# Kernel optimization log

Hardware: AMD Instinct MI355X
Metric: run time of the kernel (lower is better)

Reference implementation:

```python
import jax, jax.numpy as jnp
import numpy as np

B, S, HID, H, D, F = 8, 256, 1024, 16, 64, 64
BASE_LR = 0.1
MAX_STEPS = 4
EPS = 1e-5


def _ln(x, g, b):
    mu = jnp.mean(x, axis=-1, keepdims=True)
    var = jnp.var(x, axis=-1, keepdims=True)
    return (x - mu) * jax.lax.rsqrt(var + EPS) * g + b


def setup_inputs() -> dict:
    key = jax.random.key(0)
    ks = jax.random.split(key, 10)
    n = lambda i, shape, s=0.02: jax.random.normal(ks[i], shape, jnp.float32) * s
    return {
        "x": jax.random.normal(ks[0], (B, S, HID), jnp.float32),
        "wq": n(1, (HID, HID)),
        "wk": n(2, (HID, HID)),
        "wv": n(3, (HID, HID)),
        "fw_w1": n(4, (H, D, F), 0.05),
        "fw_b1": jnp.zeros((H, F), jnp.float32),
        "fw_w2": n(5, (H, F, D), 0.05),
        "fw_b2": jnp.zeros((H, D), jnp.float32),
        "fw_ln_g": jnp.ones((H, D), jnp.float32),
        "fw_ln_b": jnp.zeros((H, D), jnp.float32),
        "loss_w": n(6, (D, D)),
        "loss_b": jnp.zeros((D,), jnp.float32),
        "ttt_g": jnp.ones((H, D), jnp.float32),
        "ttt_b": jnp.zeros((H, D), jnp.float32),
        "wo": n(7, (HID, HID)),
        "wg": n(8, (HID, HID)),
        "pn_g": jnp.ones((HID,), jnp.float32),
        "pn_b": jnp.zeros((HID,), jnp.float32),
    }


def _fw_apply(p, kx):
    # per-head fast-weight MLP: kx (B,H,D) -> (B,H,D)
    w1, b1, w2, b2, lg, lb = p
    h = jax.nn.gelu(jnp.einsum('bhd,hdf->bhf', kx, w1) + b1)
    o = jnp.einsum('bhf,hfd->bhd', h, w2) + b2
    return _ln(o, lg, lb)


def _forward(x, wq, wk, wv, fw_w1, fw_b1, fw_w2, fw_b2, fw_ln_g, fw_ln_b,
             loss_w, loss_b, ttt_g, ttt_b, wo, wg, pn_g, pn_b):
    # projections (torch Linear with W stored as (in,out) here: y = x @ W)
    q = (x @ wq).reshape(B, S, H, D)
    k = (x @ wk).reshape(B, S, H, D)
    v = (x @ wv).reshape(B, S, H, D)
    # scan over tokens: xs shaped (S, B, H, D)
    qs = jnp.swapaxes(q, 0, 1)
    ks_ = jnp.swapaxes(k, 0, 1)
    vs = jnp.swapaxes(v, 0, 1)

    def token_step(p, qkv):
        q_t, k_t, v_t = qkv  # (B,H,D) each
        target = v_t - k_t

        def loss_fn(pp):
            z = _fw_apply(pp, k_t)
            pred = jnp.einsum('bhd,de->bhe', z, loss_w) + loss_b
            return jnp.mean((pred - target) ** 2)

        for _ in range(MAX_STEPS):
            g = jax.grad(loss_fn)(p)
            p = jax.tree.map(lambda a, gg: a - BASE_LR * gg, p, g)
        z = _fw_apply(p, k_t)
        z = _ln(z, ttt_g, ttt_b)  # per-head post-TTT LayerNorm
        return p, q_t + z

    p0 = (fw_w1, fw_b1, fw_w2, fw_b2, fw_ln_g, fw_ln_b)
    _, outs = jax.lax.scan(token_step, p0, (qs, ks_, vs))
    out = jnp.swapaxes(outs, 0, 1).reshape(B, S, HID)
    gated = jax.nn.gelu(x @ wg) * _ln(out, pn_g, pn_b)
    return gated @ wo


def reference(x, wq, wk, wv, fw_w1, fw_b1, fw_w2, fw_b2, fw_ln_g, fw_ln_b,
              loss_w, loss_b, ttt_g, ttt_b, wo, wg, pn_g, pn_b):
    return _forward(x, wq, wk, wv, fw_w1, fw_b1, fw_w2, fw_b2, fw_ln_g, fw_ln_b,
                    loss_w, loss_b, ttt_g, ttt_b, wo, wg, pn_g, pn_b)
```

## Files before the change

### kernel.cpp

```cpp
#include <hip/hip_runtime.h>

#define Bv 8
#define Sv 256
#define Hv 16
#define Dv 64
#define LR 0.1f
#define SCALE (2.0f / 8192.0f)

using bf16x8 = __attribute__((ext_vector_type(8))) short;
using bf16x4 = __attribute__((ext_vector_type(4))) short;
using f32x4  = __attribute__((ext_vector_type(4))) float;
#define MFMA16(A, B, C) __builtin_amdgcn_mfma_f32_16x16x32_bf16(A, B, C, 0, 0, 0)

constexpr int U_W1T = 0;
constexpr int U_W2T = 8704;
constexpr int U_W2R = 17408;
constexpr int U_G   = 26112;
constexpr int U_LwR = 34816;
constexpr int U_K   = 43520;
constexpr int U_H   = 45696;
constexpr int U_Z   = 47872;
constexpr int U_TG  = 50048;
constexpr int U_DO  = 52224;
constexpr int U_KT  = 54400;
constexpr int U_HT  = 55424;
constexpr int U_DOT = 56448;
constexpr int U_DAT = 57472;
constexpr int F_BASE = 29248;
constexpr int F_O   = F_BASE;
constexpr int F_XH  = F_BASE + 544;
constexpr int F_GD  = F_XH + 544;
constexpr int F_TGL = F_GD + 544;
constexpr int F_B1  = F_TGL + 544;
constexpr int F_B2  = F_B1 + 64;
constexpr int F_LG  = F_B2 + 64;
constexpr int F_LB  = F_LG + 64;
constexpr int F_C1  = F_LB + 64;
constexpr int F_TGm = F_C1 + 64;
constexpr int F_TBm = F_TGm + 64;
constexpr int F_RSTD = F_TBm + 64;
constexpr int U_KG  = (F_RSTD + 8) * 2;
constexpr int U_HT2 = U_KG + 256;
constexpr int LDS_BYTES = (U_HT2 + 1024) * 2;

__device__ __forceinline__ short bf_rn(float v) {
    unsigned u = __float_as_uint(v);
    unsigned r = u + 0x7fffu + ((u >> 16) & 1u);
    return (short)(r >> 16);
}
__device__ __forceinline__ void cvt1(float v, short &hi, short &lo) {
    hi = bf_rn(v);
    float hf = __uint_as_float(((unsigned)(unsigned short)hi) << 16);
    lo = bf_rn(v - hf);
}
__device__ __forceinline__ float bf2f(short u) {
    return __uint_as_float(((unsigned)(unsigned short)u) << 16);
}
__device__ __forceinline__ unsigned cvtpk(float a, float b) {
    unsigned r;
    asm("v_cvt_pk_bf16_f32 %0, %1, %2" : "=v"(r) : "v"(a), "v"(b));
    return r;
}
__device__ __forceinline__ void cvt2(float a, float b, unsigned &hw,
                                     unsigned &lw) {
    hw = cvtpk(a, b);
    float ra = a - __uint_as_float(hw << 16);
    float rb = b - __uint_as_float(hw & 0xffff0000u);
    lw = cvtpk(ra, rb);
}
template <int CTRL>
__device__ __forceinline__ float dpp_add(float v) {
    int s = __builtin_amdgcn_update_dpp(0, __float_as_int(v), CTRL, 0xF, 0xF,
                                        true);
    return v + __int_as_float(s);
}
__device__ __forceinline__ float red32(float v) {
    v = dpp_add<0xB1>(v);
    v = dpp_add<0x4E>(v);
    v = dpp_add<0x124>(v);
    v = dpp_add<0x128>(v);
    v += __shfl_xor(v, 16);
    return v;
}
__device__ __forceinline__ float fast_tanh(float u) {
    u = fminf(fmaxf(u, -10.f), 10.f);
    float e = __expf(2.0f * u);
    return (e - 1.0f) / (e + 1.0f);
}
__device__ __forceinline__ void gelu_both(float x, float &g, float &dg) {
    const float C0 = 0.7978845608028654f, A0 = 0.044715f;
    float x2 = x * x;
    float u = C0 * x * (1.0f + A0 * x2);
    float t = fast_tanh(u);
    g = 0.5f * x * (1.0f + t);
    float du = C0 * (1.0f + 3.0f * A0 * x2);
    dg = 0.5f * (1.0f + t) + 0.5f * x * (1.0f - t * t) * du;
}
__device__ __forceinline__ float gelu_f(float x) {
    const float C0 = 0.7978845608028654f, A0 = 0.044715f;
    float u = C0 * x * (1.0f + A0 * x * x);
    return 0.5f * x * (1.0f + fast_tanh(u));
}

__device__ __forceinline__ f32x4 mm64(const unsigned short *Ap,
                                      const unsigned short *Bp,
                                      int w, int c, int q) {
    const unsigned short *ar = Ap + c * 136 + 8 * q;
    const unsigned short *br = Bp + (16 * w + c) * 136 + 8 * q;
    bf16x8 ah0 = *(const bf16x8 *)(ar);
    bf16x8 al0 = *(const bf16x8 *)(ar + 64);
    bf16x8 bh0 = *(const bf16x8 *)(br);
    bf16x8 bl0 = *(const bf16x8 *)(br + 64);
    bf16x8 ah1 = *(const bf16x8 *)(ar + 32);
    bf16x8 al1 = *(const bf16x8 *)(ar + 96);
    bf16x8 bh1 = *(const bf16x8 *)(br + 32);
    bf16x8 bl1 = *(const bf16x8 *)(br + 96);
    f32x4 x0 = {0.f, 0.f, 0.f, 0.f}, x1 = {0.f, 0.f, 0.f, 0.f};
    x0 = MFMA16(ah0, bh0, x0); x1 = MFMA16(ah1, bh1, x1);
    x0 = MFMA16(al0, bh0, x0); x1 = MFMA16(al1, bh1, x1);
    x0 = MFMA16(ah0, bl0, x0); x1 = MFMA16(ah1, bl1, x1);
    x0 = MFMA16(al0, bl0, x0); x1 = MFMA16(al1, bl1, x1);
    return x0 + x1;
}

__device__ __forceinline__ void updW2(const bf16x8 *a4, bf16x8 b,
                                      unsigned short *WT, int w, int c,
                                      int q) {
    unsigned short *p0 = &WT[(16 * w + c) * 136 + 4 * q];
    uint2 oh[4], ol[4];
#pragma unroll
    for (int mt = 0; mt < 4; ++mt) {
        oh[mt] = *(uint2 *)(p0 + 16 * mt);
        ol[mt] = *(uint2 *)(p0 + 16 * mt + 64);
    }
    f32x4 g[4];
#pragma unroll
    for (int mt = 0; mt < 4; ++mt) {
        f32x4 z = {0.f, 0.f, 0.f, 0.f};
        g[mt] = MFMA16(a4[mt], b, z);
    }
#pragma unroll
    for (int mt = 0; mt < 4; ++mt) {
        float v0 = __uint_as_float(oh[mt].x << 16) +
                   __uint_as_float(ol[mt].x << 16) - LR * g[mt][0];
        float v1 = __uint_as_float(oh[mt].x & 0xffff0000u) +
                   __uint_as_float(ol[mt].x & 0xffff0000u) - LR * g[mt][1];
        float v2 = __uint_as_float(oh[mt].y << 16) +
                   __uint_as_float(ol[mt].y << 16) - LR * g[mt][2];
        float v3 = __uint_as_float(oh[mt].y & 0xffff0000u) +
                   __uint_as_float(ol[mt].y & 0xffff0000u) - LR * g[mt][3];
        unsigned nh0, nl0, nh1, nl1;
        cvt2(v0, v1, nh0, nl0);
        cvt2(v2, v3, nh1, nl1);
        uint2 nh, nl;
        nh.x = nh0; nh.y = nh1;
        nl.x = nl0; nl.y = nl1;
        *(uint2 *)(p0 + 16 * mt) = nh;
        *(uint2 *)(p0 + 16 * mt + 64) = nl;
    }
}

__global__ __launch_bounds__(256) void ttt_scan(
    const float *__restrict__ q_g, const float *__restrict__ k_g,
    const float *__restrict__ v_g, float *__restrict__ out_g,
    const float *__restrict__ fw_w1, const float *__restrict__ fw_b1,
    const float *__restrict__ fw_w2, const float *__restrict__ fw_b2,
    const float *__restrict__ fw_lng, const float *__restrict__ fw_lnb,
    const float *__restrict__ loss_w, const float *__restrict__ loss_bv,
    const float *__restrict__ ttt_gv, const float *__restrict__ ttt_bv) {
    extern __shared__ char smem[];
    unsigned short *us = (unsigned short *)smem;
    float *fs = (float *)smem;

    unsigned short *W1T = us + U_W1T, *W2T = us + U_W2T, *W2R = us + U_W2R;
    unsigned short *Gp = us + U_G, *LwR = us + U_LwR;
    unsigned short *Kp = us + U_K, *Hp = us + U_H, *Zp = us + U_Z;
    unsigned short *TGp = us + U_TG, *DOp = us + U_DO;
    unsigned short *KT = us + U_KT, *HT0 = us + U_HT;
    unsigned short *DOT = us + U_DOT, *DAT = us + U_DAT;
    unsigned short *KgT = us + U_KG, *HT1 = us + U_HT2;
    float *o_s = fs + F_O, *xh_s = fs + F_XH;
    float *b2_s = fs + F_B2, *lg_s = fs + F_LG;
    float *lb_s = fs + F_LB, *c1_s = fs + F_C1;
    float *tG_s = fs + F_TGm, *tB_s = fs + F_TBm, *rstd_s = fs + F_RSTD;

    const int h = blockIdx.x, tid = threadIdx.x;
    const int w = tid >> 6, lane = tid & 63, c = lane & 15, q = lane >> 4;
    const int bb = tid >> 5, j0 = (tid & 31) * 2;

    for (int i = tid; i < 4096; i += 256) {
        int r = i >> 6, cc = i & 63;
        short hi, lo;
        cvt1(fw_w1[h * 4096 + i], hi, lo);
        W1T[cc * 136 + r] = (unsigned short)hi;
        W1T[cc * 136 + 64 + r] = (unsigned short)lo;
        cvt1(fw_w2[h * 4096 + i], hi, lo);
        W2T[cc * 136 + r] = (unsigned short)hi;
        W2T[cc * 136 + 64 + r] = (unsigned short)lo;
        W2R[r * 136 + cc] = (unsigned short)hi;
        W2R[r * 136 + 64 + cc] = (unsigned short)lo;
        cvt1(loss_w[i], hi, lo);
        LwR[r * 136 + cc] = (unsigned short)hi;
        LwR[r * 136 + 64 + cc] = (unsigned short)lo;
    }
    for (int i = tid; i < 5 * 8 * 128; i += 256) {
        int a = i / 128, u = i % 128;
        int arr = a >> 3, row = 8 + (a & 7);
        unsigned short *base = (arr == 0) ? Kp : (arr == 1) ? Hp
                              : (arr == 2) ? Zp : (arr == 3) ? TGp : DOp;
        base[row * 136 + u] = 0;
    }
    __syncthreads();
#pragma unroll 1
    for (int mt = 0; mt < 4; ++mt) {
        f32x4 g = mm64(LwR + 16 * 136 * mt, LwR, w, c, q);
#pragma unroll
        for (int r = 0; r < 4; ++r) {
            short hi, lo;
            cvt1(g[r], hi, lo);
            int dr = 16 * mt + 4 * q + r, dc = 16 * w + c;
            Gp[dr * 136 + dc] = (unsigned short)hi;
            Gp[dr * 136 + 64 + dc] = (unsigned short)lo;
        }
    }
    if (tid < 64) {
        b2_s[tid] = fw_b2[h * 64 + tid];
        lg_s[tid] = fw_lng[h * 64 + tid];
        lb_s[tid] = fw_lnb[h * 64 + tid];
        tG_s[tid] = ttt_gv[h * 64 + tid];
        tB_s[tid] = ttt_bv[h * 64 + tid];
        float c1 = 0.f;
        for (int e = 0; e < 64; ++e) c1 += loss_bv[e] * loss_w[tid * 64 + e];
        c1_s[tid] = c1;
    }

    float2 pk, pv, pq, q_cur;
    {
        int idx = ((bb * Sv + 0) * Hv + h) * Dv + j0;
        float2 k0 = *(const float2 *)&k_g[idx];
        float2 v0 = *(const float2 *)&v_g[idx];
        q_cur = *(const float2 *)&q_g[idx];
        unsigned khw, klw;
        cvt2(k0.x, k0.y, khw, klw);
        *(unsigned *)&Kp[bb * 136 + j0] = khw;
        *(unsigned *)&Kp[bb * 136 + 64 + j0] = klw;
        KT[j0 * 16 + bb] = (unsigned short)khw;
        KT[j0 * 16 + 8 + bb] = (unsigned short)klw;
        KT[(j0 + 1) * 16 + bb] = (unsigned short)(khw >> 16);
        KT[(j0 + 1) * 16 + 8 + bb] = (unsigned short)(klw >> 16);
        unsigned thw, tlw;
        cvt2(v0.x - k0.x, v0.y - k0.y, thw, tlw);
        *(unsigned *)&TGp[bb * 136 + j0] = thw;
        *(unsigned *)&TGp[bb * 136 + 64 + j0] = tlw;
    }
    float b1_r = (q < 2) ? fw_b1[h * 64 + 16 * w + c] : 0.f;
    __syncthreads();
    float c1_r = c1_s[16 * w + c];
    f32x4 gd_r = {0.f, 0.f, 0.f, 0.f};
    f32x4 tgl_r = {0.f, 0.f, 0.f, 0.f};

#pragma unroll 1
    for (int t = 0; t < Sv; ++t) {
        if (t + 1 < Sv) {
            int idx2 = ((bb * Sv + t + 1) * Hv + h) * Dv + j0;
            pk = *(const float2 *)&k_g[idx2];
            pv = *(const float2 *)&v_g[idx2];
            pq = *(const float2 *)&q_g[idx2];
        }

        f32x4 acc1 = mm64(Kp, W1T, w, c, q);
        {
            f32x4 a2 = mm64(TGp, LwR, w, c, q);
            if (q < 2) {
#pragma unroll
                for (int r = 0; r < 4; ++r) tgl_r[r] = a2[r] - c1_r;
            }
        }
        if (w == 0) {
            f32x4 kg = mm64(Kp, Kp, 0, c, q);
            if (q < 2) {
#pragma unroll
                for (int r = 0; r < 4; ++r) {
                    short hi, lo;
                    cvt1(-LR * kg[r], hi, lo);
                    KgT[c * 16 + 4 * q + r] = (unsigned short)hi;
                    KgT[c * 16 + 8 + 4 * q + r] = (unsigned short)lo;
                }
            }
        }
        if (q < 2) {
            int col = 16 * w + c;
            float gv[4];
#pragma unroll
            for (int r = 0; r < 4; ++r) {
                float g, dg;
                gelu_both(acc1[r] + b1_r, g, dg);
                gv[r] = g;
                gd_r[r] = dg;
            }
            unsigned h01, l01, h23, l23;
            cvt2(gv[0], gv[1], h01, l01);
            cvt2(gv[2], gv[3], h23, l23);
            Hp[(4 * q + 0) * 136 + col] = (unsigned short)h01;
            Hp[(4 * q + 1) * 136 + col] = (unsigned short)(h01 >> 16);
            Hp[(4 * q + 2) * 136 + col] = (unsigned short)h23;
            Hp[(4 * q + 3) * 136 + col] = (unsigned short)(h23 >> 16);
            Hp[(4 * q + 0) * 136 + 64 + col] = (unsigned short)l01;
            Hp[(4 * q + 1) * 136 + 64 + col] = (unsigned short)(l01 >> 16);
            Hp[(4 * q + 2) * 136 + 64 + col] = (unsigned short)l23;
            Hp[(4 * q + 3) * 136 + 64 + col] = (unsigned short)(l23 >> 16);
            uint2 hh, hl;
            hh.x = h01; hh.y = h23;
            hl.x = l01; hl.y = l23;
            *(uint2 *)&HT0[col * 16 + 4 * q] = hh;
            *(uint2 *)&HT0[col * 16 + 8 + 4 * q] = hl;
        }
        __syncthreads();

#pragma unroll 1
        for (int step = 0; step < 4; ++step) {
            const unsigned short *HTr = (step & 1) ? HT1 : HT0;
            unsigned short *HTw = (step & 1) ? HT0 : HT1;
            f32x4 acc = mm64(Hp, W2T, w, c, q);
            if (q < 2) {
                float bias = b2_s[16 * w + c];
#pragma unroll
                for (int r = 0; r < 4; ++r)
                    o_s[(4 * q + r) * 68 + 16 * w + c] = acc[r] + bias;
            }
            __syncthreads();
            float xh0_r, xh1_r;
            {
                float2 xv = *(const float2 *)&o_s[bb * 68 + j0];
                float mu = red32(xv.x + xv.y) * (1.f / 64.f);
                float d0 = xv.x - mu, d1 = xv.y - mu;
                float var = red32(d0 * d0 + d1 * d1) * (1.f / 64.f);
                float rs = rsqrtf(var + 1e-5f);
                float xh0 = d0 * rs, xh1 = d1 * rs;
                float2 xw; xw.x = xh0; xw.y = xh1;
                *(float2 *)&xh_s[bb * 68 + j0] = xw;
                float z0 = xh0 * lg_s[j0] + lb_s[j0];
                float z1 = xh1 * lg_s[j0 + 1] + lb_s[j0 + 1];
                unsigned zh, zl;
                cvt2(z0, z1, zh, zl);
                *(unsigned *)&Zp[bb * 136 + j0] = zh;
                *(unsigned *)&Zp[bb * 136 + 64 + j0] = zl;
                if ((tid & 31) == 0) rstd_s[bb] = rs;
                xh0_r = xh0; xh1_r = xh1;
            }
            __syncthreads();
            acc = mm64(Zp, Gp, w, c, q);
            if (q < 2) {
                int col = 16 * w + c;
#pragma unroll
                for (int r = 0; r < 4; ++r)
                    o_s[(4 * q + r) * 68 + col] = (acc[r] - tgl_r[r]) * SCALE;
            }
            __syncthreads();
            {
                float2 dzv = *(const float2 *)&o_s[bb * 68 + j0];
                float dxh0 = dzv.x * lg_s[j0], dxh1 = dzv.y * lg_s[j0 + 1];
                float S1 = red32(dxh0 + dxh1) * (1.f / 64.f);
                float S2 = red32(dxh0 * xh0_r + dxh1 * xh1_r) * (1.f / 64.f);
                float rs = rstd_s[bb];
                float do0 = rs * (dxh0 - S1 - xh0_r * S2);
                float do1 = rs * (dxh1 - S1 - xh1_r * S2);
                unsigned dh, dl;
                cvt2(do0, do1, dh, dl);
                *(unsigned *)&DOp[bb * 136 + j0] = dh;
                *(unsigned *)&DOp[bb * 136 + 64 + j0] = dl;
                DOT[j0 * 16 + bb] = (unsigned short)dh;
                DOT[j0 * 16 + 8 + bb] = (unsigned short)dl;
                DOT[(j0 + 1) * 16 + bb] = (unsigned short)(dh >> 16);
                DOT[(j0 + 1) * 16 + 8 + bb] = (unsigned short)(dl >> 16);
            }
            __syncthreads();
            bf16x8 zf8;
#pragma unroll
            for (int j = 0; j < 8; ++j) zf8[j] = 0;
            bf16x8 aK[4], aH[4], aD[4];
#pragma unroll
            for (int mt = 0; mt < 4; ++mt) {
                aK[mt] = *(const bf16x8 *)&KT[(16 * mt + c) * 16 + (q & 1) * 8];
                aH[mt] = *(const bf16x8 *)&HTr[(16 * mt + c) * 16 + (q & 1) * 8];
                aD[mt] = *(const bf16x8 *)&DOT[(16 * mt + c) * 16 + (q & 1) * 8];
            }
            bf16x8 bDO = zf8, bHT = zf8;
            if (q < 2) {
                bDO = *(const bf16x8 *)&DOT[(16 * w + c) * 16];
                bHT = *(const bf16x8 *)&HTr[(16 * w + c) * 16];
            } else if (q == 2) {
                bDO = *(const bf16x8 *)&DOT[(16 * w + c) * 16 + 8];
                bHT = *(const bf16x8 *)&HTr[(16 * w + c) * 16 + 8];
            }
            bf16x8 aKg = *(const bf16x8 *)&KgT[c * 16 + (q & 1) * 8];
            acc = mm64(DOp, W2R, w, c, q);
            {
                float b1sum = 0.f;
                if (q < 2) {
                    int col = 16 * w + c;
                    float da0 = acc[0] * gd_r[0];
                    float da1 = acc[1] * gd_r[1];
                    float da2 = acc[2] * gd_r[2];
                    float da3 = acc[3] * gd_r[3];
                    b1sum = da0 + da1 + da2 + da3;
                    unsigned h01, l01, h23, l23;
                    cvt2(da0, da1, h01, l01);
                    cvt2(da2, da3, h23, l23);
                    uint2 th, tl;
                    th.x = h01; th.y = h23;
                    tl.x = l01; tl.y = l23;
                    *(uint2 *)&DAT[col * 16 + 4 * q] = th;
                    *(uint2 *)&DAT[col * 16 + 8 + 4 * q] = tl;
                }
                b1sum += __shfl_xor(b1sum, 16);
                bf16x8 bDA = zf8;
                if (q < 2)
                    bDA = *(const bf16x8 *)&DAT[(16 * w + c) * 16];
                else if (q == 2)
                    bDA = *(const bf16x8 *)&DAT[(16 * w + c) * 16 + 8];
                updW2(aK, bDA, W1T, w, c, q);
                updW2(aH, bDO, W2T, w, c, q);
                updW2(aD, bHT, W2R, w, c, q);
                if (w == 2) {
                    bf16x8 oh_ = *(const bf16x8 *)&DOT[lane * 16];
                    bf16x8 ol_ = *(const bf16x8 *)&DOT[lane * 16 + 8];
                    float db2 = 0.f;
#pragma unroll
                    for (int j = 0; j < 8; ++j)
                        db2 += bf2f(oh_[j]) + bf2f(ol_[j]);
                    b2_s[lane] -= LR * db2;
                } else if (w == 3) {
                    float dlb = 0.f, dlg = 0.f;
#pragma unroll
                    for (int b = 0; b < 8; ++b) {
                        float dzv = o_s[b * 68 + lane];
                        dlb += dzv;
                        dlg += dzv * xh_s[b * 68 + lane];
                    }
                    lb_s[lane] -= LR * dlb;
                    lg_s[lane] -= LR * dlg;
                }
                acc1 = MFMA16(aKg, bDA, acc1);
                b1_r -= LR * b1sum;
                if (q < 2) {
                    int col = 16 * w + c;
                    if (step < 3) {
                        float gv[4];
#pragma unroll
                        for (int r = 0; r < 4; ++r) {
                            float g, dg;
                            gelu_both(acc1[r] + b1_r, g, dg);
                            gv[r] = g;
                            gd_r[r] = dg;
                        }
                        unsigned h01, l01, h23, l23;
                        cvt2(gv[0], gv[1], h01, l01);
                        cvt2(gv[2], gv[3], h23, l23);
                        Hp[(4 * q + 0) * 136 + col] = (unsigned short)h01;
                        Hp[(4 * q + 1) * 136 + col] = (unsigned short)(h01 >> 16);
                        Hp[(4 * q + 2) * 136 + col] = (unsigned short)h23;
                        Hp[(4 * q + 3) * 136 + col] = (unsigned short)(h23 >> 16);
                        Hp[(4 * q + 0) * 136 + 64 + col] = (unsigned short)l01;
                        Hp[(4 * q + 1) * 136 + 64 + col] = (unsigned short)(l01 >> 16);
                        Hp[(4 * q + 2) * 136 + 64 + col] = (unsigned short)l23;
                        Hp[(4 * q + 3) * 136 + 64 + col] = (unsigned short)(l23 >> 16);
                        uint2 hh, hl;
                        hh.x = h01; hh.y = h23;
                        hl.x = l01; hl.y = l23;
                        *(uint2 *)&HTw[col * 16 + 4 * q] = hh;
                        *(uint2 *)&HTw[col * 16 + 8 + 4 * q] = hl;
                    } else {
                        float gv[4];
#pragma unroll
                        for (int r = 0; r < 4; ++r)
                            gv[r] = gelu_f(acc1[r] + b1_r);
                        unsigned h01, l01, h23, l23;
                        cvt2(gv[0], gv[1], h01, l01);
                        cvt2(gv[2], gv[3], h23, l23);
                        Hp[(4 * q + 0) * 136 + col] = (unsigned short)h01;
                        Hp[(4 * q + 1) * 136 + col] = (unsigned short)(h01 >> 16);
                        Hp[(4 * q + 2) * 136 + col] = (unsigned short)h23;
                        Hp[(4 * q + 3) * 136 + col] = (unsigned short)(h23 >> 16);
                        Hp[(4 * q + 0) * 136 + 64 + col] = (unsigned short)l01;
                        Hp[(4 * q + 1) * 136 + 64 + col] = (unsigned short)(l01 >> 16);
                        Hp[(4 * q + 2) * 136 + 64 + col] = (unsigned short)l23;
                        Hp[(4 * q + 3) * 136 + 64 + col] = (unsigned short)(l23 >> 16);
                    }
                }
            }
            __syncthreads();
        }

        f32x4 acc = mm64(Hp, W2T, w, c, q);
        if (q < 2) {
            float bias = b2_s[16 * w + c];
#pragma unroll
            for (int r = 0; r < 4; ++r)
                o_s[(4 * q + r) * 68 + 16 * w + c] = acc[r] + bias;
        }
        if (t + 1 < Sv) {
            unsigned khw, klw;
            cvt2(pk.x, pk.y, khw, klw);
            *(unsigned *)&Kp[bb * 136 + j0] = khw;
            *(unsigned *)&Kp[bb * 136 + 64 + j0] = klw;
            KT[j0 * 16 + bb] = (unsigned short)khw;
            KT[j0 * 16 + 8 + bb] = (unsigned short)klw;
            KT[(j0 + 1) * 16 + bb] = (unsigned short)(khw >> 16);
            KT[(j0 + 1) * 16 + 8 + bb] = (unsigned short)(klw >> 16);
            unsigned thw, tlw;
            cvt2(pv.x - pk.x, pv.y - pk.y, thw, tlw);
            *(unsigned *)&TGp[bb * 136 + j0] = thw;
            *(unsigned *)&TGp[bb * 136 + 64 + j0] = tlw;
        }
        __syncthreads();
        {
            float2 xv = *(const float2 *)&o_s[bb * 68 + j0];
            float mu = red32(xv.x + xv.y) * (1.f / 64.f);
            float d0 = xv.x - mu, d1 = xv.y - mu;
            float var = red32(d0 * d0 + d1 * d1) * (1.f / 64.f);
            float rs = rsqrtf(var + 1e-5f);
            float z0 = d0 * rs * lg_s[j0] + lb_s[j0];
            float z1 = d1 * rs * lg_s[j0 + 1] + lb_s[j0 + 1];
            float mu2 = red32(z0 + z1) * (1.f / 64.f);
            float e0 = z0 - mu2, e1 = z1 - mu2;
            float var2 = red32(e0 * e0 + e1 * e1) * (1.f / 64.f);
            float rs2 = rsqrtf(var2 + 1e-5f);
            float z20 = e0 * rs2 * tG_s[j0] + tB_s[j0];
            float z21 = e1 * rs2 * tG_s[j0 + 1] + tB_s[j0 + 1];
            int idx = ((bb * Sv + t) * Hv + h) * Dv + j0;
            float2 ov;
            ov.x = q_cur.x + z20;
            ov.y = q_cur.y + z21;
            *(float2 *)&out_g[idx] = ov;
            q_cur = pq;
        }
    }
}

__global__ __launch_bounds__(256) void gemm_f32(
    const float *__restrict__ A, const float *__restrict__ B,
    float *__restrict__ C, const float *__restrict__ gate_ln,
    int M, int N, int K, int mode) {
    __shared__ float As[16][68];
    __shared__ float Bs[16][64];
    const int tid = threadIdx.x;
    const int tx = tid & 15, ty = tid >> 4;
    const int bm = blockIdx.y * 64, bn = blockIdx.x * 64;

    float acc[4][4] = {};
    for (int k0 = 0; k0 < K; k0 += 16) {
        {
            int r = tid >> 2, kk = (tid & 3) * 4;
            float4 av = *(const float4 *)(A + (long)(bm + r) * K + k0 + kk);
            As[kk + 0][r] = av.x;
            As[kk + 1][r] = av.y;
            As[kk + 2][r] = av.z;
            As[kk + 3][r] = av.w;
            int rr = tid >> 4, cc = (tid & 15) * 4;
            float4 bv = *(const float4 *)(B + (long)(k0 + rr) * N + bn + cc);
            *(float4 *)&Bs[rr][cc] = bv;
        }
        __syncthreads();
#pragma unroll
        for (int kk = 0; kk < 16; ++kk) {
            float4 a4 = *(float4 *)&As[kk][ty * 4];
            float4 b4 = *(float4 *)&Bs[kk][tx * 4];
            float a[4] = {a4.x, a4.y, a4.z, a4.w};
            float b[4] = {b4.x, b4.y, b4.z, b4.w};
#pragma unroll
            for (int i = 0; i < 4; ++i)
#pragma unroll
                for (int j = 0; j < 4; ++j) acc[i][j] += a[i] * b[j];
        }
        __syncthreads();
    }
#pragma unroll
    for (int i = 0; i < 4; ++i) {
        int row = bm + ty * 4 + i;
        float4 out;
        float v[4];
#pragma unroll
        for (int j = 0; j < 4; ++j) {
            float val = acc[i][j];
            if (mode == 1) {
                int col = bn + tx * 4 + j;
                val = gelu_f(val) * gate_ln[(long)row * N + col];
            }
            v[j] = val;
        }
        out.x = v[0]; out.y = v[1]; out.z = v[2]; out.w = v[3];
        *(float4 *)(C + (long)row * N + bn + tx * 4) = out;
    }
}

__global__ __launch_bounds__(256) void row_ln(const float *__restrict__ in,
                                              float *__restrict__ out,
                                              const float *__restrict__ g,
                                              const float *__restrict__ b) {
    __shared__ float sred[4], s2red[4];
    const int row = blockIdx.x;
    const int tid = threadIdx.x;
    const float *x = in + (long)row * 1024;
    float4 v = *(const float4 *)(x + tid * 4);
    float s = v.x + v.y + v.z + v.w;
    float s2 = v.x * v.x + v.y * v.y + v.z * v.z + v.w * v.w;
#pragma unroll
    for (int m = 1; m <= 32; m <<= 1) {
        s += __shfl_xor(s, m);
        s2 += __shfl_xor(s2, m);
    }
    if ((tid & 63) == 0) {
        sred[tid >> 6] = s;
        s2red[tid >> 6] = s2;
    }
    __syncthreads();
    float S = sred[0] + sred[1] + sred[2] + sred[3];
    float S2 = s2red[0] + s2red[1] + s2red[2] + s2red[3];
    float mu = S * (1.f / 1024.f);
    float var = S2 * (1.f / 1024.f) - mu * mu;
    float rs = rsqrtf(var + 1e-5f);
    float o[4] = {v.x, v.y, v.z, v.w};
    float4 ov;
    float r[4];
#pragma unroll
    for (int i = 0; i < 4; ++i) {
        int col = tid * 4 + i;
        r[i] = (o[i] - mu) * rs * g[col] + b[col];
    }
    ov.x = r[0]; ov.y = r[1]; ov.z = r[2]; ov.w = r[3];
    *(float4 *)(out + (long)row * 1024 + tid * 4) = ov;
}

extern "C" void kernel_launch(void *const *d_in, const int *in_sizes, int n_in,
                              void *d_out, int out_size, void *d_ws,
                              size_t ws_size, hipStream_t stream) {
    const float *x = (const float *)d_in[0];
    const float *wq = (const float *)d_in[1];
    const float *wk = (const float *)d_in[2];
    const float *wv = (const float *)d_in[3];
    const float *fw_w1 = (const float *)d_in[4];
    const float *fw_b1 = (const float *)d_in[5];
    const float *fw_w2 = (const float *)d_in[6];
    const float *fw_b2 = (const float *)d_in[7];
    const float *fw_lng = (const float *)d_in[8];
    const float *fw_lnb = (const float *)d_in[9];
    const float *loss_w = (const float *)d_in[10];
    const float *loss_b = (const float *)d_in[11];
    const float *ttt_g = (const float *)d_in[12];
    const float *ttt_b = (const float *)d_in[13];
    const float *wo = (const float *)d_in[14];
    const float *wg = (const float *)d_in[15];
    const float *pn_g = (const float *)d_in[16];
    const float *pn_b = (const float *)d_in[17];

    const long MAT = 2048L * 1024L;
    float *q_ws = (float *)d_ws;
    float *k_ws = q_ws + MAT;
    float *v_ws = k_ws + MAT;
    float *out_ws = v_ws + MAT;
    float *ln_ws = k_ws;
    float *gated_ws = v_ws;

    dim3 gg(1024 / 64, 2048 / 64), bt(256);
    hipLaunchKernelGGL(gemm_f32, gg, bt, 0, stream, x, wq, q_ws,
                       (const float *)nullptr, 2048, 1024, 1024, 0);
    hipLaunchKernelGGL(gemm_f32, gg, bt, 0, stream, x, wk, k_ws,
                       (const float *)nullptr, 2048, 1024, 1024, 0);
    hipLaunchKernelGGL(gemm_f32, gg, bt, 0, stream, x, wv, v_ws,
                       (const float *)nullptr, 2048, 1024, 1024, 0);

    (void)hipFuncSetAttribute((const void *)ttt_scan,
                              hipFuncAttributeMaxDynamicSharedMemorySize,
                              LDS_BYTES);
    hipLaunchKernelGGL(ttt_scan, dim3(16), dim3(256), LDS_BYTES, stream,
                       q_ws, k_ws, v_ws, out_ws, fw_w1, fw_b1, fw_w2, fw_b2,
                       fw_lng, fw_lnb, loss_w, loss_b, ttt_g, ttt_b);

    hipLaunchKernelGGL(row_ln, dim3(2048), dim3(256), 0, stream, out_ws, ln_ws,
                       pn_g, pn_b);
    hipLaunchKernelGGL(gemm_f32, gg, bt, 0, stream, x, wg, gated_ws, ln_ws,
                       2048, 1024, 1024, 1);
    hipLaunchKernelGGL(gemm_f32, gg, bt, 0, stream, gated_ws, wo,
                       (float *)d_out, (const float *)nullptr, 2048, 1024,
                       1024, 0);
}
```

Before: 4.236 ms.

## Keep fast-weight masters in fp32 registers and feed LN outputs to MFMA from registers

Each thread now holds its slice of the fast weights (W1, W2, W2 transposed) as fp32 master copies in registers. Weight updates no longer read back and recombine the hi/lo bf16 pairs from shared memory. The layer-norm forward and backward are recomputed per lane in the MFMA A-fragment layout, so Z and dO are passed straight to the matmuls from registers. This removes the Zp/DOp shared round trips and two barriers per step. In exchange it adds register pressure, which may lower occupancy or cause spills, and duplicates the LN work across waves.

```diff
diff --git a/kernel.cpp b/kernel.cpp
--- a/kernel.cpp
+++ b/kernel.cpp
@@ -10,6 +10,7 @@
 using bf16x8 = __attribute__((ext_vector_type(8))) short;
 using bf16x4 = __attribute__((ext_vector_type(4))) short;
 using f32x4  = __attribute__((ext_vector_type(4))) float;
+using u32x4  = __attribute__((ext_vector_type(4))) unsigned;
 #define MFMA16(A, B, C) __builtin_amdgcn_mfma_f32_16x16x32_bf16(A, B, C, 0, 0, 0)
 
 constexpr int U_W1T = 0;
@@ -123,35 +124,42 @@
     return x0 + x1;
 }
 
-__device__ __forceinline__ void updW2(const bf16x8 *a4, bf16x8 b,
-                                      unsigned short *WT, int w, int c,
-                                      int q) {
-    unsigned short *p0 = &WT[(16 * w + c) * 136 + 4 * q];
-    uint2 oh[4], ol[4];
-#pragma unroll
-    for (int mt = 0; mt < 4; ++mt) {
-        oh[mt] = *(uint2 *)(p0 + 16 * mt);
-        ol[mt] = *(uint2 *)(p0 + 16 * mt + 64);
-    }
+__device__ __forceinline__ f32x4 mm64_regA(bf16x8 ah0, bf16x8 ah1,
+                                           bf16x8 al0, bf16x8 al1,
+                                           const unsigned short *Bp,
+                                           int w, int c, int q) {
+    const unsigned short *br = Bp + (16 * w + c) * 136 + 8 * q;
+    bf16x8 bh0 = *(const bf16x8 *)(br);
+    bf16x8 bl0 = *(const bf16x8 *)(br + 64);
+    bf16x8 bh1 = *(const bf16x8 *)(br + 32);
+    bf16x8 bl1 = *(const bf16x8 *)(br + 96);
+    f32x4 x0 = {0.f, 0.f, 0.f, 0.f}, x1 = {0.f, 0.f, 0.f, 0.f};
+    x0 = MFMA16(ah0, bh0, x0); x1 = MFMA16(ah1, bh1, x1);
+    x0 = MFMA16(al0, bh0, x0); x1 = MFMA16(al1, bh1, x1);
+    x0 = MFMA16(ah0, bl0, x0); x1 = MFMA16(ah1, bl1, x1);
+    x0 = MFMA16(al0, bl0, x0); x1 = MFMA16(al1, bl1, x1);
+    return x0 + x1;
+}
+
+__device__ __forceinline__ void updW3(const bf16x8 *a4, bf16x8 b,
+                                      float (&m)[16], unsigned short *WT,
+                                      int w, int c, int q) {
     f32x4 g[4];
 #pragma unroll
     for (int mt = 0; mt < 4; ++mt) {
         f32x4 z = {0.f, 0.f, 0.f, 0.f};
         g[mt] = MFMA16(a4[mt], b, z);
     }
+    unsigned short *p0 = &WT[(16 * w + c) * 136 + 4 * q];
 #pragma unroll
     for (int mt = 0; mt < 4; ++mt) {
-        float v0 = __uint_as_float(oh[mt].x << 16) +
-                   __uint_as_float(ol[mt].x << 16) - LR * g[mt][0];
-        float v1 = __uint_as_float(oh[mt].x & 0xffff0000u) +
-                   __uint_as_float(ol[mt].x & 0xffff0000u) - LR * g[mt][1];
-        float v2 = __uint_as_float(oh[mt].y << 16) +
-                   __uint_as_float(ol[mt].y << 16) - LR * g[mt][2];
-        float v3 = __uint_as_float(oh[mt].y & 0xffff0000u) +
-                   __uint_as_float(ol[mt].y & 0xffff0000u) - LR * g[mt][3];
+        m[mt * 4 + 0] -= LR * g[mt][0];
+        m[mt * 4 + 1] -= LR * g[mt][1];
+        m[mt * 4 + 2] -= LR * g[mt][2];
+        m[mt * 4 + 3] -= LR * g[mt][3];
         unsigned nh0, nl0, nh1, nl1;
-        cvt2(v0, v1, nh0, nl0);
-        cvt2(v2, v3, nh1, nl1);
+        cvt2(m[mt * 4 + 0], m[mt * 4 + 1], nh0, nl0);
+        cvt2(m[mt * 4 + 2], m[mt * 4 + 3], nh1, nl1);
         uint2 nh, nl;
         nh.x = nh0; nh.y = nh1;
         nl.x = nl0; nl.y = nl1;
@@ -179,10 +187,10 @@
     unsigned short *KT = us + U_KT, *HT0 = us + U_HT;
     unsigned short *DOT = us + U_DOT, *DAT = us + U_DAT;
     unsigned short *KgT = us + U_KG, *HT1 = us + U_HT2;
-    float *o_s = fs + F_O, *xh_s = fs + F_XH;
+    float *o_s = fs + F_O, *xh_s = fs + F_XH, *dz_s = fs + F_GD;
     float *b2_s = fs + F_B2, *lg_s = fs + F_LG;
     float *lb_s = fs + F_LB, *c1_s = fs + F_C1;
-    float *tG_s = fs + F_TGm, *tB_s = fs + F_TBm, *rstd_s = fs + F_RSTD;
+    float *tG_s = fs + F_TGm, *tB_s = fs + F_TBm;
 
     const int h = blockIdx.x, tid = threadIdx.x;
     const int w = tid >> 6, lane = tid & 63, c = lane & 15, q = lane >> 4;
@@ -209,6 +217,18 @@
         unsigned short *base = (arr == 0) ? Kp : (arr == 1) ? Hp
                               : (arr == 2) ? Zp : (arr == 3) ? TGp : DOp;
         base[row * 136 + u] = 0;
+    }
+    float w1m[16], w2m[16], w2rm[16];
+#pragma unroll
+    for (int mt = 0; mt < 4; ++mt) {
+#pragma unroll
+        for (int r = 0; r < 4; ++r) {
+            int el = 16 * mt + 4 * q + r;
+            int row = 16 * w + c;
+            w1m[mt * 4 + r] = fw_w1[h * 4096 + el * 64 + row];
+            w2m[mt * 4 + r] = fw_w2[h * 4096 + el * 64 + row];
+            w2rm[mt * 4 + r] = fw_w2[h * 4096 + row * 64 + el];
+        }
     }
     __syncthreads();
 #pragma unroll 1
@@ -329,73 +349,165 @@
                     o_s[(4 * q + r) * 68 + 16 * w + c] = acc[r] + bias;
             }
             __syncthreads();
-            float xh0_r, xh1_r;
+
+            float xh0[8], xh1[8], lgr0[8], lgr1[8], rstd_r;
             {
-                float2 xv = *(const float2 *)&o_s[bb * 68 + j0];
-                float mu = red32(xv.x + xv.y) * (1.f / 64.f);
-                float d0 = xv.x - mu, d1 = xv.y - mu;
-                float var = red32(d0 * d0 + d1 * d1) * (1.f / 64.f);
-                float rs = rsqrtf(var + 1e-5f);
-                float xh0 = d0 * rs, xh1 = d1 * rs;
-                float2 xw; xw.x = xh0; xw.y = xh1;
-                *(float2 *)&xh_s[bb * 68 + j0] = xw;
-                float z0 = xh0 * lg_s[j0] + lb_s[j0];
-                float z1 = xh1 * lg_s[j0 + 1] + lb_s[j0 + 1];
-                unsigned zh, zl;
-                cvt2(z0, z1, zh, zl);
-                *(unsigned *)&Zp[bb * 136 + j0] = zh;
-                *(unsigned *)&Zp[bb * 136 + 64 + j0] = zl;
-                if ((tid & 31) == 0) rstd_s[bb] = rs;
-                xh0_r = xh0; xh1_r = xh1;
+                const bool rok = (c < 8);
+                const float *orow = &o_s[c * 68 + 8 * q];
+                float4 z4 = {0.f, 0.f, 0.f, 0.f};
+                float4 a0 = rok ? *(const float4 *)(orow) : z4;
+                float4 a1 = rok ? *(const float4 *)(orow + 4) : z4;
+                float4 a2_ = rok ? *(const float4 *)(orow + 32) : z4;
+                float4 a3 = rok ? *(const float4 *)(orow + 36) : z4;
+                float o0[8] = {a0.x, a0.y, a0.z, a0.w, a1.x, a1.y, a1.z, a1.w};
+                float o1[8] = {a2_.x, a2_.y, a2_.z, a2_.w,
+                               a3.x, a3.y, a3.z, a3.w};
+                float s = 0.f;
+#pragma unroll
+                for (int j = 0; j < 8; ++j) s += o0[j] + o1[j];
+                s += __shfl_xor(s, 16);
+                s += __shfl_xor(s, 32);
+                float mu = s * (1.f / 64.f);
+                float sq = 0.f;
+#pragma unroll
+                for (int j = 0; j < 8; ++j) {
+                    xh0[j] = o0[j] - mu;
+                    xh1[j] = o1[j] - mu;
+                    sq += xh0[j] * xh0[j] + xh1[j] * xh1[j];
+                }
+                sq += __shfl_xor(sq, 16);
+                sq += __shfl_xor(sq, 32);
+                rstd_r = rsqrtf(sq * (1.f / 64.f) + 1e-5f);
+#pragma unroll
+                for (int j = 0; j < 8; ++j) {
+                    xh0[j] *= rstd_r;
+                    xh1[j] *= rstd_r;
+                }
+                float4 g0 = *(const float4 *)&lg_s[8 * q];
+                float4 g1 = *(const float4 *)&lg_s[8 * q + 4];
+                float4 g2 = *(const float4 *)&lg_s[8 * q + 32];
+                float4 g3 = *(const float4 *)&lg_s[8 * q + 36];
+                lgr0[0] = g0.x; lgr0[1] = g0.y; lgr0[2] = g0.z; lgr0[3] = g0.w;
+                lgr0[4] = g1.x; lgr0[5] = g1.y; lgr0[6] = g1.z; lgr0[7] = g1.w;
+                lgr1[0] = g2.x; lgr1[1] = g2.y; lgr1[2] = g2.z; lgr1[3] = g2.w;
+                lgr1[4] = g3.x; lgr1[5] = g3.y; lgr1[6] = g3.z; lgr1[7] = g3.w;
+                float4 e0 = *(const float4 *)&lb_s[8 * q];
+                float4 e1 = *(const float4 *)&lb_s[8 * q + 4];
+                float4 e2 = *(const float4 *)&lb_s[8 * q + 32];
+                float4 e3 = *(const float4 *)&lb_s[8 * q + 36];
+                float lbr0[8] = {e0.x, e0.y, e0.z, e0.w,
+                                 e1.x, e1.y, e1.z, e1.w};
+                float lbr1[8] = {e2.x, e2.y, e2.z, e2.w,
+                                 e3.x, e3.y, e3.z, e3.w};
+                float zz0[8], zz1[8];
+#pragma unroll
+                for (int j = 0; j < 8; ++j) {
+                    zz0[j] = xh0[j] * lgr0[j] + lbr0[j];
+                    zz1[j] = xh1[j] * lgr1[j] + lbr1[j];
+                }
+                if (w == 0 && rok) {
+                    float4 x4;
+                    x4.x = xh0[0]; x4.y = xh0[1]; x4.z = xh0[2]; x4.w = xh0[3];
+                    *(float4 *)&xh_s[c * 68 + 8 * q] = x4;
+                    x4.x = xh0[4]; x4.y = xh0[5]; x4.z = xh0[6]; x4.w = xh0[7];
+                    *(float4 *)&xh_s[c * 68 + 8 * q + 4] = x4;
+                    x4.x = xh1[0]; x4.y = xh1[1]; x4.z = xh1[2]; x4.w = xh1[3];
+                    *(float4 *)&xh_s[c * 68 + 8 * q + 32] = x4;
+                    x4.x = xh1[4]; x4.y = xh1[5]; x4.z = xh1[6]; x4.w = xh1[7];
+                    *(float4 *)&xh_s[c * 68 + 8 * q + 36] = x4;
+                }
+                u32x4 H0, L0, H1, L1;
+#pragma unroll
+                for (int p = 0; p < 4; ++p) {
+                    unsigned hh, ll;
+                    cvt2(zz0[2 * p], zz0[2 * p + 1], hh, ll);
+                    H0[p] = rok ? hh : 0u;
+                    L0[p] = rok ? ll : 0u;
+                    cvt2(zz1[2 * p], zz1[2 * p + 1], hh, ll);
+                    H1[p] = rok ? hh : 0u;
+                    L1[p] = rok ? ll : 0u;
+                }
+                bf16x8 zh0 = __builtin_bit_cast(bf16x8, H0);
+                bf16x8 zh1 = __builtin_bit_cast(bf16x8, H1);
+                bf16x8 zl0 = __builtin_bit_cast(bf16x8, L0);
+                bf16x8 zl1 = __builtin_bit_cast(bf16x8, L1);
+                acc = mm64_regA(zh0, zh1, zl0, zl1, Gp, w, c, q);
+                if (q < 2) {
+                    int col = 16 * w + c;
+#pragma unroll
+                    for (int r = 0; r < 4; ++r)
+                        dz_s[(4 * q + r) * 68 + col] =
+                            (acc[r] - tgl_r[r]) * SCALE;
+                }
             }
             __syncthreads();
-            acc = mm64(Zp, Gp, w, c, q);
-            if (q < 2) {
-                int col = 16 * w + c;
-#pragma unroll
-                for (int r = 0; r < 4; ++r)
-                    o_s[(4 * q + r) * 68 + col] = (acc[r] - tgl_r[r]) * SCALE;
-            }
-            __syncthreads();
+
             {
-                float2 dzv = *(const float2 *)&o_s[bb * 68 + j0];
-                float dxh0 = dzv.x * lg_s[j0], dxh1 = dzv.y * lg_s[j0 + 1];
-                float S1 = red32(dxh0 + dxh1) * (1.f / 64.f);
-                float S2 = red32(dxh0 * xh0_r + dxh1 * xh1_r) * (1.f / 64.f);
-                float rs = rstd_s[bb];
-                float do0 = rs * (dxh0 - S1 - xh0_r * S2);
-                float do1 = rs * (dxh1 - S1 - xh1_r * S2);
-                unsigned dh, dl;
-                cvt2(do0, do1, dh, dl);
-                *(unsigned *)&DOp[bb * 136 + j0] = dh;
-                *(unsigned *)&DOp[bb * 136 + 64 + j0] = dl;
-                DOT[j0 * 16 + bb] = (unsigned short)dh;
-                DOT[j0 * 16 + 8 + bb] = (unsigned short)dl;
-                DOT[(j0 + 1) * 16 + bb] = (unsigned short)(dh >> 16);
-                DOT[(j0 + 1) * 16 + 8 + bb] = (unsigned short)(dl >> 16);
-            }
-            __syncthreads();
-            bf16x8 zf8;
-#pragma unroll
-            for (int j = 0; j < 8; ++j) zf8[j] = 0;
-            bf16x8 aK[4], aH[4], aD[4];
-#pragma unroll
-            for (int mt = 0; mt < 4; ++mt) {
-                aK[mt] = *(const bf16x8 *)&KT[(16 * mt + c) * 16 + (q & 1) * 8];
-                aH[mt] = *(const bf16x8 *)&HTr[(16 * mt + c) * 16 + (q & 1) * 8];
-                aD[mt] = *(const bf16x8 *)&DOT[(16 * mt + c) * 16 + (q & 1) * 8];
-            }
-            bf16x8 bDO = zf8, bHT = zf8;
-            if (q < 2) {
-                bDO = *(const bf16x8 *)&DOT[(16 * w + c) * 16];
-                bHT = *(const bf16x8 *)&HTr[(16 * w + c) * 16];
-            } else if (q == 2) {
-                bDO = *(const bf16x8 *)&DOT[(16 * w + c) * 16 + 8];
-                bHT = *(const bf16x8 *)&HTr[(16 * w + c) * 16 + 8];
-            }
-            bf16x8 aKg = *(const bf16x8 *)&KgT[c * 16 + (q & 1) * 8];
-            acc = mm64(DOp, W2R, w, c, q);
-            {
+                const bool rok = (c < 8);
+                const float *drow = &dz_s[c * 68 + 8 * q];
+                float4 z4 = {0.f, 0.f, 0.f, 0.f};
+                float4 a0 = rok ? *(const float4 *)(drow) : z4;
+                float4 a1 = rok ? *(const float4 *)(drow + 4) : z4;
+                float4 a2_ = rok ? *(const float4 *)(drow + 32) : z4;
+                float4 a3 = rok ? *(const float4 *)(drow + 36) : z4;
+                float dz0[8] = {a0.x, a0.y, a0.z, a0.w,
+                                a1.x, a1.y, a1.z, a1.w};
+                float dz1[8] = {a2_.x, a2_.y, a2_.z, a2_.w,
+                                a3.x, a3.y, a3.z, a3.w};
+                float dxh0[8], dxh1[8];
+                float s1 = 0.f, s2 = 0.f;
+#pragma unroll
+                for (int j = 0; j < 8; ++j) {
+                    dxh0[j] = dz0[j] * lgr0[j];
+                    dxh1[j] = dz1[j] * lgr1[j];
+                    s1 += dxh0[j] + dxh1[j];
+                    s2 += dxh0[j] * xh0[j] + dxh1[j] * xh1[j];
+                }
+                s1 += __shfl_xor(s1, 16);
+                s2 += __shfl_xor(s2, 16);
+                s1 += __shfl_xor(s1, 32);
+                s2 += __shfl_xor(s2, 32);
+                float S1 = s1 * (1.f / 64.f), S2 = s2 * (1.f / 64.f);
+                float do0[8], do1[8];
+#pragma unroll
+                for (int j = 0; j < 8; ++j) {
+                    do0[j] = rstd_r * (dxh0[j] - S1 - xh0[j] * S2);
+                    do1[j] = rstd_r * (dxh1[j] - S1 - xh1[j] * S2);
+                }
+                u32x4 H0, L0, H1, L1;
+#pragma unroll
+                for (int p = 0; p < 4; ++p) {
+                    unsigned hh, ll;
+                    cvt2(do0[2 * p], do0[2 * p + 1], hh, ll);
+                    H0[p] = rok ? hh : 0u;
+                    L0[p] = rok ? ll : 0u;
+                    cvt2(do1[2 * p], do1[2 * p + 1], hh, ll);
+                    H1[p] = rok ? hh : 0u;
+                    L1[p] = rok ? ll : 0u;
+                }
+                if (rok) {
+#pragma unroll
+                    for (int p = 0; p < 4; ++p) {
+                        int d0 = 8 * q + 2 * p;
+                        DOT[d0 * 16 + c] = (unsigned short)H0[p];
+                        DOT[d0 * 16 + 8 + c] = (unsigned short)L0[p];
+                        DOT[(d0 + 1) * 16 + c] = (unsigned short)(H0[p] >> 16);
+                        DOT[(d0 + 1) * 16 + 8 + c] =
+                            (unsigned short)(L0[p] >> 16);
+                        int d1 = d0 + 32;
+                        DOT[d1 * 16 + c] = (unsigned short)H1[p];
+                        DOT[d1 * 16 + 8 + c] = (unsigned short)L1[p];
+                        DOT[(d1 + 1) * 16 + c] = (unsigned short)(H1[p] >> 16);
+                        DOT[(d1 + 1) * 16 + 8 + c] =
+                            (unsigned short)(L1[p] >> 16);
+                    }
+                }
+                bf16x8 dh0 = __builtin_bit_cast(bf16x8, H0);
+                bf16x8 dh1 = __builtin_bit_cast(bf16x8, H1);
+                bf16x8 dl0 = __builtin_bit_cast(bf16x8, L0);
+                bf16x8 dl1 = __builtin_bit_cast(bf16x8, L1);
+                acc = mm64_regA(dh0, dh1, dl0, dl1, W2R, w, c, q);
+
                 float b1sum = 0.f;
                 if (q < 2) {
                     int col = 16 * w + c;
@@ -414,14 +526,34 @@
                     *(uint2 *)&DAT[col * 16 + 8 + 4 * q] = tl;
                 }
                 b1sum += __shfl_xor(b1sum, 16);
-                bf16x8 bDA = zf8;
-                if (q < 2)
+
+                bf16x8 zf8;
+#pragma unroll
+                for (int j = 0; j < 8; ++j) zf8[j] = 0;
+                bf16x8 aK[4], aH[4], aD[4];
+#pragma unroll
+                for (int mt = 0; mt < 4; ++mt) {
+                    aK[mt] = *(const bf16x8 *)
+                        &KT[(16 * mt + c) * 16 + (q & 1) * 8];
+                    aH[mt] = *(const bf16x8 *)
+                        &HTr[(16 * mt + c) * 16 + (q & 1) * 8];
+                    aD[mt] = *(const bf16x8 *)
+                        &DOT[(16 * mt + c) * 16 + (q & 1) * 8];
+                }
+                bf16x8 bDO = zf8, bHT = zf8, bDA = zf8;
+                if (q < 2) {
+                    bDO = *(const bf16x8 *)&DOT[(16 * w + c) * 16];
+                    bHT = *(const bf16x8 *)&HTr[(16 * w + c) * 16];
                     bDA = *(const bf16x8 *)&DAT[(16 * w + c) * 16];
-                else if (q == 2)
+                } else if (q == 2) {
+                    bDO = *(const bf16x8 *)&DOT[(16 * w + c) * 16 + 8];
+                    bHT = *(const bf16x8 *)&HTr[(16 * w + c) * 16 + 8];
                     bDA = *(const bf16x8 *)&DAT[(16 * w + c) * 16 + 8];
-                updW2(aK, bDA, W1T, w, c, q);
-                updW2(aH, bDO, W2T, w, c, q);
-                updW2(aD, bHT, W2R, w, c, q);
+                }
+                bf16x8 aKg = *(const bf16x8 *)&KgT[c * 16 + (q & 1) * 8];
+                updW3(aK, bDA, w1m, W1T, w, c, q);
+                updW3(aH, bDO, w2m, W2T, w, c, q);
+                updW3(aD, bHT, w2rm, W2R, w, c, q);
                 if (w == 2) {
                     bf16x8 oh_ = *(const bf16x8 *)&DOT[lane * 16];
                     bf16x8 ol_ = *(const bf16x8 *)&DOT[lane * 16 + 8];
@@ -434,7 +566,7 @@
                     float dlb = 0.f, dlg = 0.f;
 #pragma unroll
                     for (int b = 0; b < 8; ++b) {
-                        float dzv = o_s[b * 68 + lane];
+                        float dzv = dz_s[b * 68 + lane];
                         dlb += dzv;
                         dlg += dzv * xh_s[b * 68 + lane];
                     }
```

Result: slower. 4.514 ms (+6.6%).

## Keep fp32 master weights in registers, shuffle DA operand, drop lo*lo MFMA

Applied to the files above, without the earlier changes.

Fast-weight matrices W1, W2 and W2R now keep fp32 master copies in registers per thread, so each gradient update no longer reads the bf16 hi/lo pairs back from LDS. The DA operand is passed between lanes with shuffles instead of a round trip through LDS, which removes an LDS buffer and its traffic. The lo*lo term of the split-bf16 matmul is dropped, and the LayerNorm statistics use one-pass sum and sum-of-squares reductions so both can run together. Costs are 48 extra registers per thread, which can limit occupancy, and slightly lower precision from the dropped MFMA term and the one-pass variance.

```diff
diff --git a/kernel.cpp b/kernel.cpp
--- a/kernel.cpp
+++ b/kernel.cpp
@@ -10,6 +10,7 @@
 using bf16x8 = __attribute__((ext_vector_type(8))) short;
 using bf16x4 = __attribute__((ext_vector_type(4))) short;
 using f32x4  = __attribute__((ext_vector_type(4))) float;
+using u32x4  = __attribute__((ext_vector_type(4))) unsigned;
 #define MFMA16(A, B, C) __builtin_amdgcn_mfma_f32_16x16x32_bf16(A, B, C, 0, 0, 0)
 
 constexpr int U_W1T = 0;
@@ -119,39 +120,28 @@
     x0 = MFMA16(ah0, bh0, x0); x1 = MFMA16(ah1, bh1, x1);
     x0 = MFMA16(al0, bh0, x0); x1 = MFMA16(al1, bh1, x1);
     x0 = MFMA16(ah0, bl0, x0); x1 = MFMA16(ah1, bl1, x1);
-    x0 = MFMA16(al0, bl0, x0); x1 = MFMA16(al1, bl1, x1);
     return x0 + x1;
 }
 
-__device__ __forceinline__ void updW2(const bf16x8 *a4, bf16x8 b,
-                                      unsigned short *WT, int w, int c,
-                                      int q) {
-    unsigned short *p0 = &WT[(16 * w + c) * 136 + 4 * q];
-    uint2 oh[4], ol[4];
-#pragma unroll
-    for (int mt = 0; mt < 4; ++mt) {
-        oh[mt] = *(uint2 *)(p0 + 16 * mt);
-        ol[mt] = *(uint2 *)(p0 + 16 * mt + 64);
-    }
+__device__ __forceinline__ void updW3(const bf16x8 *a4, bf16x8 b,
+                                      float (&m)[16], unsigned short *WT,
+                                      int w, int c, int q) {
     f32x4 g[4];
 #pragma unroll
     for (int mt = 0; mt < 4; ++mt) {
         f32x4 z = {0.f, 0.f, 0.f, 0.f};
         g[mt] = MFMA16(a4[mt], b, z);
     }
+    unsigned short *p0 = &WT[(16 * w + c) * 136 + 4 * q];
 #pragma unroll
     for (int mt = 0; mt < 4; ++mt) {
-        float v0 = __uint_as_float(oh[mt].x << 16) +
-                   __uint_as_float(ol[mt].x << 16) - LR * g[mt][0];
-        float v1 = __uint_as_float(oh[mt].x & 0xffff0000u) +
-                   __uint_as_float(ol[mt].x & 0xffff0000u) - LR * g[mt][1];
-        float v2 = __uint_as_float(oh[mt].y << 16) +
-                   __uint_as_float(ol[mt].y << 16) - LR * g[mt][2];
-        float v3 = __uint_as_float(oh[mt].y & 0xffff0000u) +
-                   __uint_as_float(ol[mt].y & 0xffff0000u) - LR * g[mt][3];
+        m[mt * 4 + 0] -= LR * g[mt][0];
+        m[mt * 4 + 1] -= LR * g[mt][1];
+        m[mt * 4 + 2] -= LR * g[mt][2];
+        m[mt * 4 + 3] -= LR * g[mt][3];
         unsigned nh0, nl0, nh1, nl1;
-        cvt2(v0, v1, nh0, nl0);
-        cvt2(v2, v3, nh1, nl1);
+        cvt2(m[mt * 4 + 0], m[mt * 4 + 1], nh0, nl0);
+        cvt2(m[mt * 4 + 2], m[mt * 4 + 3], nh1, nl1);
         uint2 nh, nl;
         nh.x = nh0; nh.y = nh1;
         nl.x = nl0; nl.y = nl1;
@@ -177,7 +167,7 @@
     unsigned short *Kp = us + U_K, *Hp = us + U_H, *Zp = us + U_Z;
     unsigned short *TGp = us + U_TG, *DOp = us + U_DO;
     unsigned short *KT = us + U_KT, *HT0 = us + U_HT;
-    unsigned short *DOT = us + U_DOT, *DAT = us + U_DAT;
+    unsigned short *DOT = us + U_DOT;
     unsigned short *KgT = us + U_KG, *HT1 = us + U_HT2;
     float *o_s = fs + F_O, *xh_s = fs + F_XH;
     float *b2_s = fs + F_B2, *lg_s = fs + F_LG;
@@ -209,6 +199,18 @@
         unsigned short *base = (arr == 0) ? Kp : (arr == 1) ? Hp
                               : (arr == 2) ? Zp : (arr == 3) ? TGp : DOp;
         base[row * 136 + u] = 0;
+    }
+    float w1m[16], w2m[16], w2rm[16];
+#pragma unroll
+    for (int mt = 0; mt < 4; ++mt) {
+#pragma unroll
+        for (int r = 0; r < 4; ++r) {
+            int el = 16 * mt + 4 * q + r;
+            int row = 16 * w + c;
+            w1m[mt * 4 + r] = fw_w1[h * 4096 + el * 64 + row];
+            w2m[mt * 4 + r] = fw_w2[h * 4096 + el * 64 + row];
+            w2rm[mt * 4 + r] = fw_w2[h * 4096 + row * 64 + el];
+        }
     }
     __syncthreads();
 #pragma unroll 1
@@ -332,11 +334,12 @@
             float xh0_r, xh1_r;
             {
                 float2 xv = *(const float2 *)&o_s[bb * 68 + j0];
-                float mu = red32(xv.x + xv.y) * (1.f / 64.f);
-                float d0 = xv.x - mu, d1 = xv.y - mu;
-                float var = red32(d0 * d0 + d1 * d1) * (1.f / 64.f);
+                float s = red32(xv.x + xv.y);
+                float s2 = red32(xv.x * xv.x + xv.y * xv.y);
+                float mu = s * (1.f / 64.f);
+                float var = s2 * (1.f / 64.f) - mu * mu;
                 float rs = rsqrtf(var + 1e-5f);
-                float xh0 = d0 * rs, xh1 = d1 * rs;
+                float xh0 = (xv.x - mu) * rs, xh1 = (xv.y - mu) * rs;
                 float2 xw; xw.x = xh0; xw.y = xh1;
                 *(float2 *)&xh_s[bb * 68 + j0] = xw;
                 float z0 = xh0 * lg_s[j0] + lb_s[j0];
@@ -397,8 +400,9 @@
             acc = mm64(DOp, W2R, w, c, q);
             {
                 float b1sum = 0.f;
+                uint2 th; th.x = 0u; th.y = 0u;
+                uint2 tl; tl.x = 0u; tl.y = 0u;
                 if (q < 2) {
-                    int col = 16 * w + c;
                     float da0 = acc[0] * gd_r[0];
                     float da1 = acc[1] * gd_r[1];
                     float da2 = acc[2] * gd_r[2];
@@ -407,21 +411,28 @@
                     unsigned h01, l01, h23, l23;
                     cvt2(da0, da1, h01, l01);
                     cvt2(da2, da3, h23, l23);
-                    uint2 th, tl;
                     th.x = h01; th.y = h23;
                     tl.x = l01; tl.y = l23;
-                    *(uint2 *)&DAT[col * 16 + 4 * q] = th;
-                    *(uint2 *)&DAT[col * 16 + 8 + 4 * q] = tl;
                 }
                 b1sum += __shfl_xor(b1sum, 16);
-                bf16x8 bDA = zf8;
-                if (q < 2)
-                    bDA = *(const bf16x8 *)&DAT[(16 * w + c) * 16];
-                else if (q == 2)
-                    bDA = *(const bf16x8 *)&DAT[(16 * w + c) * 16 + 8];
-                updW2(aK, bDA, W1T, w, c, q);
-                updW2(aH, bDO, W2T, w, c, q);
-                updW2(aD, bHT, W2R, w, c, q);
+                unsigned hx0 = (unsigned)__shfl((int)th.x, c);
+                unsigned hy0 = (unsigned)__shfl((int)th.y, c);
+                unsigned hx1 = (unsigned)__shfl((int)th.x, c + 16);
+                unsigned hy1 = (unsigned)__shfl((int)th.y, c + 16);
+                unsigned lx0 = (unsigned)__shfl((int)tl.x, c);
+                unsigned ly0 = (unsigned)__shfl((int)tl.y, c);
+                unsigned lx1 = (unsigned)__shfl((int)tl.x, c + 16);
+                unsigned ly1 = (unsigned)__shfl((int)tl.y, c + 16);
+                u32x4 Bw = {0u, 0u, 0u, 0u};
+                if (q < 2) {
+                    Bw[0] = hx0; Bw[1] = hy0; Bw[2] = hx1; Bw[3] = hy1;
+                } else if (q == 2) {
+                    Bw[0] = lx0; Bw[1] = ly0; Bw[2] = lx1; Bw[3] = ly1;
+                }
+                bf16x8 bDA = __builtin_bit_cast(bf16x8, Bw);
+                updW3(aK, bDA, w1m, W1T, w, c, q);
+                updW3(aH, bDO, w2m, W2T, w, c, q);
+                updW3(aD, bHT, w2rm, W2R, w, c, q);
                 if (w == 2) {
                     bf16x8 oh_ = *(const bf16x8 *)&DOT[lane * 16];
                     bf16x8 ol_ = *(const bf16x8 *)&DOT[lane * 16 + 8];
@@ -516,18 +527,20 @@
         __syncthreads();
         {
             float2 xv = *(const float2 *)&o_s[bb * 68 + j0];
-            float mu = red32(xv.x + xv.y) * (1.f / 64.f);
-            float d0 = xv.x - mu, d1 = xv.y - mu;
-            float var = red32(d0 * d0 + d1 * d1) * (1.f / 64.f);
+            float s = red32(xv.x + xv.y);
+            float s2 = red32(xv.x * xv.x + xv.y * xv.y);
+            float mu = s * (1.f / 64.f);
+            float var = s2 * (1.f / 64.f) - mu * mu;
             float rs = rsqrtf(var + 1e-5f);
-            float z0 = d0 * rs * lg_s[j0] + lb_s[j0];
-            float z1 = d1 * rs * lg_s[j0 + 1] + lb_s[j0 + 1];
-            float mu2 = red32(z0 + z1) * (1.f / 64.f);
-            float e0 = z0 - mu2, e1 = z1 - mu2;
-            float var2 = red32(e0 * e0 + e1 * e1) * (1.f / 64.f);
+            float z0 = (xv.x - mu) * rs * lg_s[j0] + lb_s[j0];
+            float z1 = (xv.y - mu) * rs * lg_s[j0 + 1] + lb_s[j0 + 1];
+            float sb = red32(z0 + z1);
+            float s2b = red32(z0 * z0 + z1 * z1);
+            float mu2 = sb * (1.f / 64.f);
+            float var2 = s2b * (1.f / 64.f) - mu2 * mu2;
             float rs2 = rsqrtf(var2 + 1e-5f);
-            float z20 = e0 * rs2 * tG_s[j0] + tB_s[j0];
-            float z21 = e1 * rs2 * tG_s[j0 + 1] + tB_s[j0 + 1];
+            float z20 = (z0 - mu2) * rs2 * tG_s[j0] + tB_s[j0];
+            float z21 = (z1 - mu2) * rs2 * tG_s[j0 + 1] + tB_s[j0 + 1];
             int idx = ((bb * Sv + t) * Hv + h) * Dv + j0;
             float2 ov;
             ov.x = q_cur.x + z20;
```

Result: faster. 3.920 ms (-7.4%).
